# Optimization experiments

Hardware: AMD Instinct MI355X
Metric: run time of the kernel (lower is better)

The kernel has to match this reference:

```python
import jax, jax.numpy as jnp
import numpy as np
from jax import lax

D_MODEL = 1024
D_STATE = 16
D_CONV = 4
EXPAND = 2
D_INNER = EXPAND * D_MODEL           # 2048 (mamba inner)
DT_RANK = (D_MODEL + 15) // 16       # 64
D_FF = 4 * D_MODEL                   # 4096 (SwiGLU hidden)
EPS = 1e-5
B, L = 2, 2048


def setup_inputs() -> dict:
    key = jax.random.key(0)
    ks = jax.random.split(key, 16)
    s = 0.02
    inp = {
        'x': jax.random.normal(ks[0], (B, L, D_MODEL), jnp.float32),
        'norm1_w': jnp.ones((D_MODEL,), jnp.float32),
        'norm2_w': jnp.ones((D_MODEL,), jnp.float32),
        # Mamba params (torch Linear convention: y = x @ W.T)
        'in_proj_w': s * jax.random.normal(ks[1], (2 * D_INNER, D_MODEL), jnp.float32),
        'conv_w': s * jax.random.normal(ks[2], (D_INNER, 1, D_CONV), jnp.float32),
        'conv_b': jnp.zeros((D_INNER,), jnp.float32),
        'x_proj_w': s * jax.random.normal(ks[3], (DT_RANK + 2 * D_STATE, D_INNER), jnp.float32),
        'dt_proj_w': s * jax.random.normal(ks[4], (D_INNER, DT_RANK), jnp.float32),
        'dt_proj_b': jax.random.uniform(ks[5], (D_INNER,), jnp.float32, -4.0, -2.0),
        'A_log': jnp.log(jnp.broadcast_to(jnp.arange(1, D_STATE + 1, dtype=jnp.float32), (D_INNER, D_STATE))),
        'D': jnp.ones((D_INNER,), jnp.float32),
        'out_proj_w': s * jax.random.normal(ks[6], (D_MODEL, D_INNER), jnp.float32),
        # SwiGLU MLP
        'w1': s * jax.random.normal(ks[7], (D_FF, D_MODEL), jnp.float32),
        'w2': s * jax.random.normal(ks[8], (D_FF, D_MODEL), jnp.float32),
        'w3': s * jax.random.normal(ks[9], (D_MODEL, D_FF), jnp.float32),
    }
    return inp


def _rmsnorm(x, w, eps=EPS):
    return x * lax.rsqrt(jnp.mean(x * x, axis=-1, keepdims=True) + eps) * w


def _mamba(x, in_proj_w, conv_w, conv_b, x_proj_w, dt_proj_w, dt_proj_b, A_log, Dp, out_proj_w):
    # x: (B, L, d_model)
    xz = x @ in_proj_w.T                       # (B, L, 2*d_inner)
    u, z = jnp.split(xz, 2, axis=-1)           # each (B, L, d_inner)
    # causal depthwise conv1d over time
    u_nch = u.transpose(0, 2, 1)               # (B, d_inner, L)
    u_conv = lax.conv_general_dilated(
        u_nch, conv_w, window_strides=(1,), padding=[(D_CONV - 1, 0)],
        dimension_numbers=('NCH', 'OIH', 'NCH'), feature_group_count=D_INNER)
    u_conv = u_conv + conv_b[None, :, None]
    u_act = jax.nn.silu(u_conv.transpose(0, 2, 1))   # (B, L, d_inner)
    # input-dependent dt, B, C
    proj = u_act @ x_proj_w.T                  # (B, L, dt_rank + 2*d_state)
    dt_r, Bm, Cm = jnp.split(proj, [DT_RANK, DT_RANK + D_STATE], axis=-1)
    dt = jax.nn.softplus(dt_r @ dt_proj_w.T + dt_proj_b)   # (B, L, d_inner)
    A = -jnp.exp(A_log)                        # (d_inner, d_state)
    dA = jnp.exp(jnp.einsum('bld,dn->bldn', dt, A))
    dBu = jnp.einsum('bld,bln,bld->bldn', dt, Bm, u_act)
    def step(h, inputs):
        dA_t, dBu_t = inputs                   # (B, d_inner, d_state)
        h = dA_t * h + dBu_t
        return h, h
    h0 = jnp.zeros((x.shape[0], D_INNER, D_STATE), x.dtype)
    _, hs = lax.scan(step, h0, (dA.transpose(1, 0, 2, 3), dBu.transpose(1, 0, 2, 3)))
    y = jnp.einsum('lbdn,bln->bld', hs, Cm) + u_act * Dp   # (B, L, d_inner)
    y = y * jax.nn.silu(z)
    return y @ out_proj_w.T                    # (B, L, d_model)


def reference(x, norm1_w, norm2_w, in_proj_w, conv_w, conv_b, x_proj_w,
              dt_proj_w, dt_proj_b, A_log, D, out_proj_w, w1, w2, w3):
    # residual + RMSNorm + Mamba (dropout = eval-mode identity)
    h = x + _mamba(_rmsnorm(x, norm1_w), in_proj_w, conv_w, conv_b,
                   x_proj_w, dt_proj_w, dt_proj_b, A_log, D, out_proj_w)
    # residual + RMSNorm + SwiGLU MLP
    xn = _rmsnorm(h, norm2_w)
    mlp = (jax.nn.silu(xn @ w1.T) * (xn @ w2.T)) @ w3.T
    return h + mlp
```

## Files before the change

### kernel.cpp

```cpp
#include <hip/hip_runtime.h>
#include <hip/hip_bf16.h>

#define TOKS 4096
#define DM   1024
#define DI   2048
#define DST  16
#define DTR  64
#define DFF  4096
#define PROJ_LD 128

#define NC    32
#define CHUNK 64

typedef __bf16 bf16x8 __attribute__((ext_vector_type(8)));
typedef float  f32x4  __attribute__((ext_vector_type(4)));

__device__ __forceinline__ __bf16 f2bf(float f) {
  union { float f; unsigned u; } v; v.f = f;
  unsigned r = v.u + 0x7fffu + ((v.u >> 16) & 1u);
  union { unsigned short s; __bf16 b; } o; o.s = (unsigned short)(r >> 16);
  return o.b;
}
__device__ __forceinline__ float siluf(float x) { return x / (1.f + __expf(-x)); }
__device__ __forceinline__ float softplusf(float x) { return x > 20.f ? x : log1pf(__expf(x)); }

__device__ __forceinline__ void gl2lds16(const void* g, void* l) {
  __builtin_amdgcn_global_load_lds((const __attribute__((address_space(1))) void*)g,
                                   (__attribute__((address_space(3))) void*)l, 16, 0, 0);
}

struct CvtArgs {
  const float* src[5];
  __bf16*      dst[5];
  int nblk[6];
};

__global__ __launch_bounds__(256) void cvt_bf16_kernel(CvtArgs a) {
  int blk = blockIdx.x;
  int seg = 0;
#pragma unroll
  for (int s = 1; s < 5; s++) if (blk >= a.nblk[s]) seg = s;
  size_t base = (size_t)(blk - a.nblk[seg]) * 2048 + threadIdx.x * 8;
  const float* src = a.src[seg] + base;
  __bf16*      dst = a.dst[seg] + base;
  float4 v0 = *(const float4*)src;
  float4 v1 = *(const float4*)(src + 4);
  union { __bf16 b[8]; uint4 u; } t;
  t.b[0]=f2bf(v0.x); t.b[1]=f2bf(v0.y); t.b[2]=f2bf(v0.z); t.b[3]=f2bf(v0.w);
  t.b[4]=f2bf(v1.x); t.b[5]=f2bf(v1.y); t.b[6]=f2bf(v1.z); t.b[7]=f2bf(v1.w);
  *(uint4*)dst = t.u;
}

__global__ __launch_bounds__(256) void cvt_w12_kernel(const float* __restrict__ w1,
                                                      const float* __restrict__ w2,
                                                      __bf16* __restrict__ dst) {
  int blk = blockIdx.x;
  int isw2 = blk >> 11;
  int b = blk & 2047;
  int r = b * 2 + (threadIdx.x >> 7);
  int col = (threadIdx.x & 127) * 8;
  const float* src = (isw2 ? w2 : w1) + (size_t)r * DM + col;
  int dr = (r >> 4) * 32 + (r & 15) + isw2 * 16;
  float4 v0 = *(const float4*)src;
  float4 v1 = *(const float4*)(src + 4);
  union { __bf16 b[8]; uint4 u; } t;
  t.b[0]=f2bf(v0.x); t.b[1]=f2bf(v0.y); t.b[2]=f2bf(v0.z); t.b[3]=f2bf(v0.w);
  t.b[4]=f2bf(v1.x); t.b[5]=f2bf(v1.y); t.b[6]=f2bf(v1.z); t.b[7]=f2bf(v1.w);
  *(uint4*)&dst[(size_t)dr * DM + col] = t.u;
}

__global__ __launch_bounds__(256) void rmsnorm_kernel(const float* __restrict__ x,
                                                      const float* __restrict__ w,
                                                      __bf16* __restrict__ out) {
  int row = blockIdx.x;
  const float* xr = x + (size_t)row * DM;
  float4 v = ((const float4*)xr)[threadIdx.x];
  float ss = v.x*v.x + v.y*v.y + v.z*v.z + v.w*v.w;
#pragma unroll
  for (int o = 32; o > 0; o >>= 1) ss += __shfl_xor(ss, o);
  __shared__ float sred[4];
  if ((threadIdx.x & 63) == 0) sred[threadIdx.x >> 6] = ss;
  __syncthreads();
  float tot = sred[0] + sred[1] + sred[2] + sred[3];
  float scale = rsqrtf(tot * (1.f / DM) + 1e-5f);
  float4 wv = ((const float4*)w)[threadIdx.x];
  union { __bf16 b[4]; ushort4 u; } o;
  o.b[0] = f2bf(v.x * scale * wv.x);
  o.b[1] = f2bf(v.y * scale * wv.y);
  o.b[2] = f2bf(v.z * scale * wv.z);
  o.b[3] = f2bf(v.w * scale * wv.w);
  *(ushort4*)&out[(size_t)row * DM + threadIdx.x * 4] = o.u;
}

template<int BM, int EPI, int SWAP, int KK, int Z, int LDA, int LDB, int LDC>
__global__ __launch_bounds__(256, BM == 128 ? 1 : 2) void gemm2(
    const void* __restrict__ Ap, const __bf16* __restrict__ Bp,
    void* __restrict__ Cp, const void* __restrict__ auxp)
{
  constexpr int FM = BM / 32;
  constexpr int AI = BM / 64;
  constexpr int kPer = KK / Z;
  __shared__ __bf16 sA[2][BM * 32];
  __shared__ __bf16 sB[2][128 * 32];
  const int tid  = threadIdx.x;
  const int wave = tid >> 6, lane = tid & 63;
  const int bm = SWAP ? blockIdx.x : blockIdx.y;
  const int bn = SWAP ? blockIdx.y : blockIdx.x;
  const int m0 = bm * BM, n0 = bn * 128;
  const int wr = wave >> 1, wc = wave & 1;
  const int frow = lane & 15, fq = lane >> 4;

  f32x4 acc[FM][4] = {};

  const int kBeg = (Z > 1) ? blockIdx.z * kPer : 0;
  const int kEnd = kBeg + kPer;

  const int lrow = lane >> 2;
  const int lcol = (lane & 3) * 8;

  auto stage = [&](int kt, int buf) {
#pragma unroll
    for (int q = 0; q < AI; q++) {
      int idx = wave * AI + q;
      gl2lds16((const __bf16*)Ap + (size_t)(m0 + idx * 16 + lrow) * LDA + kt + lcol,
               &sA[buf][idx * 512]);
    }
#pragma unroll
    for (int q = 0; q < 2; q++) {
      int idx = wave * 2 + q;
      gl2lds16(Bp + (size_t)(n0 + idx * 16 + lrow) * LDB + kt + lcol,
               &sB[buf][idx * 512]);
    }
  };

  stage(kBeg, 0);
  int cur = 0;
  for (int kt = kBeg; kt < kEnd; kt += 32) {
    __syncthreads();

    bf16x8 afr[FM], bfr[4];
#pragma unroll
    for (int i = 0; i < FM; i++)
      afr[i] = *(const bf16x8*)&sA[cur][(wr * (BM/2) + i * 16 + frow) * 32 + fq * 8];
#pragma unroll
    for (int j = 0; j < 4; j++)
      bfr[j] = *(const bf16x8*)&sB[cur][(wc * 64 + j * 16 + frow) * 32 + fq * 8];

    if (kt + 32 < kEnd) stage(kt + 32, cur ^ 1);

#pragma unroll
    for (int i = 0; i < FM; i++)
#pragma unroll
      for (int j = 0; j < 4; j++)
        acc[i][j] = __builtin_amdgcn_mfma_f32_16x16x32_bf16(afr[i], bfr[j], acc[i][j], 0, 0, 0);
    cur ^= 1;
  }

  const float* auxf = (const float*)auxp;
#pragma unroll
  for (int i = 0; i < FM; i++) {
    int gr = m0 + wr * (BM/2) + i * 16 + fq * 4;
#pragma unroll
    for (int j = 0; j < 4; j++) {
      int gc = n0 + wc * 64 + j * 16 + frow;
#pragma unroll
      for (int r = 0; r < 4; r++) {
        float v = acc[i][j][r];
        if (EPI == 6) {
          if (j & 1) {
            int col = (n0 >> 1) + 32 * wc + 16 * (j >> 1) + frow;
            size_t off = (size_t)(gr + r) * LDC + col;
            float g = acc[i][j-1][r];
            ((__bf16*)Cp)[off] = f2bf(siluf(g) * v);
          }
        } else {
          size_t off = (size_t)(gr + r) * LDC + gc;
          if (EPI == 1) ((__bf16*)Cp)[off] = f2bf(v);
          else if (EPI == 2) ((__bf16*)Cp)[off] = f2bf(softplusf(v + auxf[gc]));
          else if (EPI == 3) ((float*)Cp)[off] = v + auxf[off];
          else if (EPI == 7)
            ((float*)Cp)[(size_t)blockIdx.z * (TOKS * PROJ_LD) + off] = v;
        }
      }
    }
  }
}

template<int EPI, int KK, int LDA, int LDB, int LDC, int GX>
__global__ __launch_bounds__(512, 2) void gemm8(
    const __bf16* __restrict__ Ap, const __bf16* __restrict__ Bp,
    void* __restrict__ Cp)
{
  constexpr int NT = KK / 64;
  static_assert(NT % 2 == 0 && NT >= 4, "KK must be a multiple of 128");
  __shared__ alignas(16) char S[131072];

  const int tid  = threadIdx.x;
  const int wid  = tid >> 6, lane = tid & 63;
  const int wr   = wid >> 2, wc = wid & 3;
  const int bid = blockIdx.y * (GX * 8) + blockIdx.x;
  const int xcd = bid & 7, idx = bid >> 3;
  const int m0 = (idx / GX) * 256;
  const int n0 = (xcd * GX + (idx % GX)) * 256;
  const int frow = lane & 15, fq = lane >> 4;
  const int cbyt = (fq * 16) ^ (((lane >> 3) & 1) << 5);
  const int srow = lane >> 2;
  const int skin = ((lane & 3) * 8) ^ (((lane >> 5) & 1) << 4);

  const unsigned sbase = (unsigned)(size_t)(__attribute__((address_space(3))) char*)S;
  const unsigned abase = sbase + (unsigned)((wr * 64 + frow) * 64 + cbyt);
  const unsigned bbase = sbase + 32768u + (unsigned)((wc * 32 + frow) * 64 + cbyt);

  f32x4 acc[2][2][4][2] = {};
  bf16x8 fA[4][2], fB0[2][2], fB1[2][2];

#define G8_SB() __builtin_amdgcn_sched_barrier(0)
#define G8_BAR() do { G8_SB(); __builtin_amdgcn_s_barrier(); G8_SB(); } while (0)
#define G8_LGKM0() do { asm volatile("s_waitcnt lgkmcnt(0)"); G8_SB(); } while (0)
#define G8_THROT() asm volatile("s_waitcnt lgkmcnt(8)")
#define G8_WAIT6() asm volatile("s_waitcnt vmcnt(6)")
#define G8_WAIT0() asm volatile("s_waitcnt vmcnt(0)")
#define G8_DSR(dst, addr, OFF)                                                 \
    asm volatile("ds_read_b128 %0, %1 offset:" OFF : "=v"(dst) : "v"(addr))

#define G8_STAGE(buf, ab, h, tile) do {                                        \
    if ((tile) < NT) {                                                         \
      const __bf16* gb = (ab) ? Bp : Ap;                                       \
      const int ld = (ab) ? LDB : LDA;                                         \
      const int r0 = ((ab) ? n0 : m0) + (h) * 128;                             \
      _Pragma("unroll")                                                        \
      for (int q = 0; q < 2; q++) {                                            \
        int p = wid * 2 + q, kk = p >> 3, r16 = p & 7;                         \
        const __bf16* src = gb + (size_t)(r0 + r16 * 16 + srow) * ld           \
                            + (tile) * 64 + kk * 32 + skin;                    \
        char* dst = S + (((buf) * 4 + (ab) * 2 + kk) << 14)                    \
                    + ((h) * 128 + r16 * 16) * 64;                             \
        gl2lds16(src, dst);                                                    \
      }                                                                        \
    }                                                                          \
  } while (0)

#define G8_READ_A(buf, mh) do {                                                \
    unsigned a_ = abase + (buf) * 65536u + (mh) * 8192u;                       \
    f32x4 t0,t1,t2,t3,t4,t5,t6,t7;                                             \
    G8_DSR(t0, a_, "0");     G8_DSR(t1, a_, "1024");                           \
    G8_DSR(t2, a_, "2048");  G8_DSR(t3, a_, "3072");                           \
    G8_DSR(t4, a_, "16384"); G8_DSR(t5, a_, "17408");                          \
    G8_DSR(t6, a_, "18432"); G8_DSR(t7, a_, "19456");                          \
    fA[0][0]=__builtin_bit_cast(bf16x8,t0); fA[1][0]=__builtin_bit_cast(bf16x8,t1); \
    fA[2][0]=__builtin_bit_cast(bf16x8,t2); fA[3][0]=__builtin_bit_cast(bf16x8,t3); \
    fA[0][1]=__builtin_bit_cast(bf16x8,t4); fA[1][1]=__builtin_bit_cast(bf16x8,t5); \
    fA[2][1]=__builtin_bit_cast(bf16x8,t6); fA[3][1]=__builtin_bit_cast(bf16x8,t7); \
  } while (0)

#define G8_READ_B(buf, nh, FB) do {                                            \
    unsigned b_ = bbase + (buf) * 65536u + (nh) * 8192u;                       \
    f32x4 t0,t1,t2,t3;                                                         \
    G8_DSR(t0, b_, "0");     G8_DSR(t1, b_, "1024");                           \
    G8_DSR(t2, b_, "16384"); G8_DSR(t3, b_, "17408");                          \
    FB[0][0]=__builtin_bit_cast(bf16x8,t0); FB[1][0]=__builtin_bit_cast(bf16x8,t1); \
    FB[0][1]=__builtin_bit_cast(bf16x8,t2); FB[1][1]=__builtin_bit_cast(bf16x8,t3); \
  } while (0)

#define G8_MFMA(mh, nh, FB) do {                                               \
    __builtin_amdgcn_s_setprio(1);                                             \
    _Pragma("unroll")                                                          \
    for (int kk = 0; kk < 2; kk++)                                             \
      _Pragma("unroll")                                                        \
      for (int fi = 0; fi < 4; fi++)                                           \
        _Pragma("unroll")                                                      \
        for (int fj = 0; fj < 2; fj++)                                         \
          acc[mh][nh][fi][fj] = __builtin_amdgcn_mfma_f32_16x16x32_bf16(       \
              fA[fi][kk], FB[fj][kk], acc[mh][nh][fi][fj], 0, 0, 0);           \
    __builtin_amdgcn_s_setprio(0);                                             \
    G8_SB();                                                                   \
  } while (0)

  G8_STAGE(0, 0, 0, 0); G8_STAGE(0, 1, 1, 0); G8_STAGE(0, 0, 1, 0); G8_STAGE(0, 1, 0, 0);
  G8_STAGE(1, 0, 0, 1); G8_STAGE(1, 1, 1, 1); G8_STAGE(1, 0, 1, 1);
  G8_SB();
  G8_WAIT6();
  G8_BAR();

  for (int it = 0; it < NT / 2; ++it) {
    const int t1 = 2 * it + 1, t2 = 2 * it + 2, t3 = 2 * it + 3;
    const bool last = (it == NT / 2 - 1);
    G8_READ_A(0, 0); G8_READ_B(0, 0, fB0);
    G8_STAGE(1, 1, 0, t1);
    G8_SB(); G8_THROT();
    G8_BAR();
    G8_LGKM0();
    G8_MFMA(0, 0, fB0);
    G8_BAR();
    G8_READ_B(0, 1, fB1);
    G8_STAGE(0, 0, 0, t2);
    G8_SB();
    G8_BAR();
    G8_LGKM0();
    G8_MFMA(0, 1, fB1);
    G8_BAR();
    G8_READ_A(0, 1);
    G8_STAGE(0, 1, 1, t2);
    G8_SB();
    G8_BAR();
    G8_LGKM0();
    G8_MFMA(1, 1, fB1);
    G8_BAR();
    G8_STAGE(0, 0, 1, t2);
    G8_SB();
    if (last) G8_WAIT0(); else G8_WAIT6();
    G8_BAR();
    G8_MFMA(1, 0, fB0);
    G8_BAR();
    G8_READ_A(1, 0); G8_READ_B(1, 0, fB0);
    G8_STAGE(0, 1, 0, t2);
    G8_SB(); G8_THROT();
    G8_BAR();
    G8_LGKM0();
    G8_MFMA(0, 0, fB0);
    G8_BAR();
    G8_READ_B(1, 1, fB1);
    G8_STAGE(1, 0, 0, t3);
    G8_SB();
    G8_BAR();
    G8_LGKM0();
    G8_MFMA(0, 1, fB1);
    G8_BAR();
    G8_READ_A(1, 1);
    G8_STAGE(1, 1, 1, t3);
    G8_SB();
    G8_BAR();
    G8_LGKM0();
    G8_MFMA(1, 1, fB1);
    G8_BAR();
    G8_STAGE(1, 0, 1, t3);
    G8_SB();
    if (!last) G8_WAIT6();
    G8_BAR();
    G8_MFMA(1, 0, fB0);
    G8_BAR();
  }

#undef G8_STAGE
#undef G8_READ_A
#undef G8_READ_B
#undef G8_MFMA
#undef G8_BAR
#undef G8_SB
#undef G8_LGKM0
#undef G8_THROT
#undef G8_WAIT6
#undef G8_WAIT0
#undef G8_DSR

#pragma unroll
  for (int mh = 0; mh < 2; mh++)
#pragma unroll
    for (int nh = 0; nh < 2; nh++)
#pragma unroll
      for (int fi = 0; fi < 4; fi++) {
        int gr = m0 + mh * 128 + wr * 64 + fi * 16 + fq * 4;
        if constexpr (EPI == 1) {
#pragma unroll
          for (int fj = 0; fj < 2; fj++) {
            int gc = n0 + nh * 128 + wc * 32 + fj * 16 + frow;
#pragma unroll
            for (int r = 0; r < 4; r++)
              ((__bf16*)Cp)[(size_t)(gr + r) * LDC + gc] = f2bf(acc[mh][nh][fi][fj][r]);
          }
        } else {
          int col = ((n0 + nh * 128 + wc * 32) >> 1) + frow;
#pragma unroll
          for (int r = 0; r < 4; r++) {
            float g = acc[mh][nh][fi][0][r];
            float v = acc[mh][nh][fi][1][r];
            ((__bf16*)Cp)[(size_t)(gr + r) * LDC + col] = f2bf(siluf(g) * v);
          }
        }
      }
}

__global__ __launch_bounds__(256) void xp_reduce_kernel(const float* __restrict__ part,
                                                        float* __restrict__ proj,
                                                        __bf16* __restrict__ projb) {
  int i = blockIdx.x * 256 + threadIdx.x;
  float4 s = ((const float4*)part)[i];
#pragma unroll
  for (int z = 1; z < 8; z++) {
    float4 v = ((const float4*)(part + (size_t)z * TOKS * PROJ_LD))[i];
    s.x += v.x; s.y += v.y; s.z += v.z; s.w += v.w;
  }
  ((float4*)proj)[i] = s;
  int c4 = i & 31;
  if (c4 < 16) {
    int tok = i >> 5;
    union { __bf16 b[4]; ushort4 u; } t;
    t.b[0]=f2bf(s.x); t.b[1]=f2bf(s.y); t.b[2]=f2bf(s.z); t.b[3]=f2bf(s.w);
    *(ushort4*)&projb[(size_t)tok * 64 + c4 * 4] = t.u;
  }
}

__global__ __launch_bounds__(256) void conv_silu_kernel(const __bf16* __restrict__ xz,
                                                        const float* __restrict__ cw,
                                                        const float* __restrict__ cb,
                                                        __bf16* __restrict__ uact) {
  int idx = blockIdx.x * 256 + threadIdx.x;
  int d8  = (idx & 255) * 8;
  int tok = idx >> 8;
  int l   = tok & 2047;
  const __bf16* up = xz + (size_t)tok * (2 * DI) + d8;
  bf16x8 u0 = {}, u1 = {}, u2 = {}, u3;
  if (l >= 3) u0 = *(const bf16x8*)(up - 3 * (2 * DI));
  if (l >= 2) u1 = *(const bf16x8*)(up - 2 * (2 * DI));
  if (l >= 1) u2 = *(const bf16x8*)(up - 1 * (2 * DI));
  u3 = *(const bf16x8*)up;
  float4 cb0 = *(const float4*)(cb + d8);
  float4 cb1 = *(const float4*)(cb + d8 + 4);
  float cbv[8] = {cb0.x, cb0.y, cb0.z, cb0.w, cb1.x, cb1.y, cb1.z, cb1.w};
  union { __bf16 b[8]; uint4 u; } res;
#pragma unroll
  for (int j = 0; j < 8; j++) {
    float4 wv = *(const float4*)(cw + (size_t)(d8 + j) * 4);
    float acc = cbv[j];
    acc += wv.x * (float)u0[j];
    acc += wv.y * (float)u1[j];
    acc += wv.z * (float)u2[j];
    acc += wv.w * (float)u3[j];
    res.b[j] = f2bf(siluf(acc));
  }
  *(uint4*)&uact[(size_t)tok * DI + d8] = res.u;
}

__global__ __launch_bounds__(64) void scan_pass1(const __bf16* __restrict__ dt,
                                                 const __bf16* __restrict__ uact,
                                                 const float* __restrict__ proj,
                                                 const float* __restrict__ A_log,
                                                 float* __restrict__ aprod,
                                                 float* __restrict__ hend) {
  int lane = threadIdx.x;
  int d = blockIdx.x * 64 + lane;
  int c = blockIdx.y, b = blockIdx.z;
  float An[16], h[16], ap[16];
  {
    const float4* a4 = (const float4*)(A_log + (size_t)d * 16);
#pragma unroll
    for (int q = 0; q < 4; q++) {
      float4 v = a4[q];
      An[q*4+0] = -__expf(v.x); An[q*4+1] = -__expf(v.y);
      An[q*4+2] = -__expf(v.z); An[q*4+3] = -__expf(v.w);
    }
  }
#pragma unroll
  for (int n = 0; n < 16; n++) { h[n] = 0.f; ap[n] = 1.f; }

  size_t tok = (size_t)b * 2048 + (size_t)c * CHUNK;
  const __bf16* dtp = dt   + tok * DI + d;
  const __bf16* up  = uact + tok * DI + d;
  const float*  pp  = proj + tok * PROJ_LD;

  for (int t = 0; t < CHUNK; t++) {
    float dtv = (float)*dtp;
    float uv  = (float)*up;
    const float4* b4 = (const float4*)(pp + 64);
    float Bv[16];
#pragma unroll
    for (int q = 0; q < 4; q++) {
      float4 v = b4[q];
      Bv[q*4+0]=v.x; Bv[q*4+1]=v.y; Bv[q*4+2]=v.z; Bv[q*4+3]=v.w;
    }
    float du = dtv * uv;
#pragma unroll
    for (int n = 0; n < 16; n++) {
      float dA = __expf(dtv * An[n]);
      ap[n] *= dA;
      h[n] = fmaf(dA, h[n], du * Bv[n]);
    }
    dtp += DI; up += DI; pp += PROJ_LD;
  }

  size_t off = ((size_t)(b * NC + c) * DI + d) * 16;
#pragma unroll
  for (int q = 0; q < 4; q++) {
    *(float4*)(hend  + off + q*4) = make_float4(h[q*4+0],  h[q*4+1],  h[q*4+2],  h[q*4+3]);
    *(float4*)(aprod + off + q*4) = make_float4(ap[q*4+0], ap[q*4+1], ap[q*4+2], ap[q*4+3]);
  }
}

__global__ __launch_bounds__(256) void scan_pass2(const float* __restrict__ aprod,
                                                  const float* __restrict__ hend,
                                                  float* __restrict__ hstart) {
  int idx = blockIdx.x * 256 + threadIdx.x;
  int b  = idx >> 13;
  int r4 = idx & 8191;
  float4 H = make_float4(0.f, 0.f, 0.f, 0.f);
  for (int c = 0; c < NC; c++) {
    size_t off = (size_t)(b * NC + c) * (DI * 16 / 4) + r4;
    ((float4*)hstart)[off] = H;
    float4 a = ((const float4*)aprod)[off];
    float4 e = ((const float4*)hend)[off];
    H.x = fmaf(a.x, H.x, e.x);
    H.y = fmaf(a.y, H.y, e.y);
    H.z = fmaf(a.z, H.z, e.z);
    H.w = fmaf(a.w, H.w, e.w);
  }
}

__global__ __launch_bounds__(64) void scan_pass3(const __bf16* __restrict__ dt,
                                                 const __bf16* __restrict__ uact,
                                                 const float* __restrict__ proj,
                                                 const __bf16* __restrict__ xz,
                                                 const float* __restrict__ A_log,
                                                 const float* __restrict__ Dp,
                                                 const float* __restrict__ hstart,
                                                 __bf16* __restrict__ y) {
  int lane = threadIdx.x;
  int d = blockIdx.x * 64 + lane;
  int c = blockIdx.y, b = blockIdx.z;
  float An[16], h[16];
  {
    const float4* a4 = (const float4*)(A_log + (size_t)d * 16);
#pragma unroll
    for (int q = 0; q < 4; q++) {
      float4 v = a4[q];
      An[q*4+0] = -__expf(v.x); An[q*4+1] = -__expf(v.y);
      An[q*4+2] = -__expf(v.z); An[q*4+3] = -__expf(v.w);
    }
  }
  {
    size_t off = ((size_t)(b * NC + c) * DI + d) * 16;
#pragma unroll
    for (int q = 0; q < 4; q++) {
      float4 v = *(const float4*)(hstart + off + q*4);
      h[q*4+0]=v.x; h[q*4+1]=v.y; h[q*4+2]=v.z; h[q*4+3]=v.w;
    }
  }
  float Dd = Dp[d];

  size_t tok = (size_t)b * 2048 + (size_t)c * CHUNK;
  const __bf16* dtp = dt   + tok * DI + d;
  const __bf16* up  = uact + tok * DI + d;
  const float*  pp  = proj + tok * PROJ_LD;
  const __bf16* zp  = xz   + tok * (2 * DI) + DI + d;
  __bf16*       yp  = y    + tok * DI + d;

  for (int t = 0; t < CHUNK; t++) {
    float dtv = (float)*dtp;
    float uv  = (float)*up;
    float zv  = (float)*zp;
    const float4* b4 = (const float4*)(pp + 64);
    float Bv[16], Cv[16];
#pragma unroll
    for (int q = 0; q < 4; q++) {
      float4 v = b4[q];
      Bv[q*4+0]=v.x; Bv[q*4+1]=v.y; Bv[q*4+2]=v.z; Bv[q*4+3]=v.w;
      float4 w = b4[q + 4];
      Cv[q*4+0]=w.x; Cv[q*4+1]=w.y; Cv[q*4+2]=w.z; Cv[q*4+3]=w.w;
    }
    float du = dtv * uv;
    float p = 0.f;
#pragma unroll
    for (int n = 0; n < 16; n++) {
      float dA = __expf(dtv * An[n]);
      h[n] = fmaf(dA, h[n], du * Bv[n]);
      p = fmaf(h[n], Cv[n], p);
    }
    *yp = f2bf((p + Dd * uv) * siluf(zv));
    dtp += DI; up += DI; pp += PROJ_LD; zp += 2 * DI; yp += DI;
  }
}

extern "C" void kernel_launch(void* const* d_in, const int* in_sizes, int n_in,
                              void* d_out, int out_size, void* d_ws, size_t ws_size,
                              hipStream_t stream) {
  const float* x        = (const float*)d_in[0];
  const float* n1w      = (const float*)d_in[1];
  const float* n2w      = (const float*)d_in[2];
  const float* in_projw = (const float*)d_in[3];
  const float* conv_w   = (const float*)d_in[4];
  const float* conv_b   = (const float*)d_in[5];
  const float* x_projw  = (const float*)d_in[6];
  const float* dt_projw = (const float*)d_in[7];
  const float* dt_projb = (const float*)d_in[8];
  const float* A_log    = (const float*)d_in[9];
  const float* Dp       = (const float*)d_in[10];
  const float* out_projw= (const float*)d_in[11];
  const float* w1       = (const float*)d_in[12];
  const float* w2       = (const float*)d_in[13];
  const float* w3       = (const float*)d_in[14];
  float* out = (float*)d_out;

  char* ws = (char*)d_ws;
  __bf16* xz   = (__bf16*)(ws + 0);
  __bf16* uact = (__bf16*)(ws + 33554432);
  float*  proj = (float*) (ws + 50331648);
  __bf16* dt   = (__bf16*)(ws + 52428800);
  __bf16* yb   = (__bf16*)(ws + 85983232);
  float*  xpp  = (float*) (ws + 85983232);
  float*  h    = (float*) (ws + 102760448);
  __bf16* xn   = (__bf16*)(ws + 119537664);
  __bf16* hid  = xz;
  __bf16* projb = (__bf16*)(ws + 102760448);
  float* aprod  = (float*)(ws + 102760448);
  float* hend   = (float*)(ws + 111149056);
  float* hstart = (float*)(ws + 119537664);
  char* wb = ws + 127926272;
  __bf16* b_in  = (__bf16*)(wb);
  __bf16* b_xp  = (__bf16*)(wb + 8388608);
  __bf16* b_dtp = (__bf16*)(wb + 8912896);
  __bf16* b_out = (__bf16*)(wb + 9175040);
  __bf16* b_w12 = (__bf16*)(wb + 13369344);
  __bf16* b_w3  = (__bf16*)(wb + 30146560);

  hipMemsetAsync(b_xp, 0, 128 * 2048 * sizeof(__bf16), stream);

  CvtArgs ca;
  const float* srcs[5] = {in_projw, x_projw, dt_projw, out_projw, w3};
  __bf16* dsts[5]      = {b_in, b_xp, b_dtp, b_out, b_w3};
  int counts[5] = {4096*1024, 96*2048, 2048*64, 1024*2048, 1024*4096};
  int acc = 0;
  for (int i = 0; i < 5; i++) { ca.src[i] = srcs[i]; ca.dst[i] = dsts[i]; ca.nblk[i] = acc; acc += counts[i] / 2048; }
  ca.nblk[5] = acc;
  cvt_bf16_kernel<<<acc, 256, 0, stream>>>(ca);
  cvt_w12_kernel<<<4096, 256, 0, stream>>>(w1, w2, b_w12);

  dim3 blk(256);
  rmsnorm_kernel<<<TOKS, 256, 0, stream>>>(x, n1w, xn);
  gemm8<1, 1024, DM, DM, 4096, 2><<<dim3(16, 16), 512, 0, stream>>>(xn, b_in, xz);
  conv_silu_kernel<<<(TOKS*DI/8)/256, 256, 0, stream>>>(xz, conv_w, conv_b, uact);
  gemm2<64,7,0, 2048,8, DI,DI,PROJ_LD><<<dim3(1,64,8), blk, 0, stream>>>(uact, b_xp, xpp, nullptr);
  xp_reduce_kernel<<<512, 256, 0, stream>>>(xpp, proj, projb);
  gemm2<128,2,0, 64,1, 64,DTR,DI><<<dim3(16,32,1), blk, 0, stream>>>(projb, b_dtp, dt, dt_projb);
  scan_pass1<<<dim3(DI/64, NC, 2), 64, 0, stream>>>(dt, uact, proj, A_log, aprod, hend);
  scan_pass2<<<64, 256, 0, stream>>>(aprod, hend, hstart);
  scan_pass3<<<dim3(DI/64, NC, 2), 64, 0, stream>>>(dt, uact, proj, xz, A_log, Dp, hstart, yb);
  gemm2<64,3,1, 2048,1, DI,DI,DM><<<dim3(64,8,1), blk, 0, stream>>>(yb, b_out, h, x);
  rmsnorm_kernel<<<TOKS, 256, 0, stream>>>(h, n2w, xn);
  gemm8<6, 1024, DM, DM, DFF, 4><<<dim3(32, 16), 512, 0, stream>>>(xn, b_w12, hid);
  gemm2<64,3,1, 4096,1, DFF,DFF,DM><<<dim3(64,8,1), blk, 0, stream>>>(hid, b_w3, out, h);

  (void)in_sizes; (void)n_in; (void)out_size; (void)ws_size;
}
```

Measured before the change: 524.4 us.

## Add 4-stage async-LDS pipelined GEMM for out_proj and w3 residual GEMMs

After: 509.5 us. -2.8%, faster.

```diff
diff --git a/kernel.cpp b/kernel.cpp
--- a/kernel.cpp
+++ b/kernel.cpp
@@ -166,21 +166,108 @@
 #pragma unroll
       for (int r = 0; r < 4; r++) {
         float v = acc[i][j][r];
-        if (EPI == 6) {
-          if (j & 1) {
-            int col = (n0 >> 1) + 32 * wc + 16 * (j >> 1) + frow;
-            size_t off = (size_t)(gr + r) * LDC + col;
-            float g = acc[i][j-1][r];
-            ((__bf16*)Cp)[off] = f2bf(siluf(g) * v);
-          }
-        } else {
-          size_t off = (size_t)(gr + r) * LDC + gc;
-          if (EPI == 1) ((__bf16*)Cp)[off] = f2bf(v);
-          else if (EPI == 2) ((__bf16*)Cp)[off] = f2bf(softplusf(v + auxf[gc]));
-          else if (EPI == 3) ((float*)Cp)[off] = v + auxf[off];
-          else if (EPI == 7)
-            ((float*)Cp)[(size_t)blockIdx.z * (TOKS * PROJ_LD) + off] = v;
-        }
+        size_t off = (size_t)(gr + r) * LDC + gc;
+        if (EPI == 1) ((__bf16*)Cp)[off] = f2bf(v);
+        else if (EPI == 2) ((__bf16*)Cp)[off] = f2bf(softplusf(v + auxf[gc]));
+        else if (EPI == 3) ((float*)Cp)[off] = v + auxf[off];
+        else if (EPI == 7)
+          ((float*)Cp)[(size_t)blockIdx.z * (TOKS * PROJ_LD) + off] = v;
+      }
+    }
+  }
+}
+
+template<int KK, int LDA, int LDB, int LDC>
+__global__ __launch_bounds__(256, 2) void gemm2d(
+    const __bf16* __restrict__ Ap, const __bf16* __restrict__ Bp,
+    float* __restrict__ Cp, const float* __restrict__ auxp)
+{
+  constexpr int NSTEP = KK / 32;
+  static_assert(NSTEP % 4 == 0 && NSTEP >= 8, "KK must be mult of 128");
+  __shared__ alignas(16) char S2[49152];
+  const int tid  = threadIdx.x;
+  const int wave = tid >> 6, lane = tid & 63;
+  const int m0 = blockIdx.x * 64, n0 = blockIdx.y * 128;
+  const int wr = wave >> 1, wc = wave & 1;
+  const int frow = lane & 15, fq = lane >> 4;
+  const int lrow = lane >> 2, lcol = (lane & 3) * 8;
+
+  f32x4 acc[2][4] = {};
+
+  const unsigned s2 = (unsigned)(size_t)(__attribute__((address_space(3))) char*)S2;
+  const unsigned aAddr = s2 + (unsigned)((wr * 32 + frow) * 64 + fq * 16);
+  const unsigned bAddr = s2 + 16384u + (unsigned)((wc * 64 + frow) * 64 + fq * 16);
+
+  auto stage = [&](int tile, int buf) {
+    gl2lds16(Ap + (size_t)(m0 + wave * 16 + lrow) * LDA + tile * 32 + lcol,
+             S2 + buf * 4096 + wave * 1024);
+#pragma unroll
+    for (int q = 0; q < 2; q++) {
+      int idx = wave * 2 + q;
+      gl2lds16(Bp + (size_t)(n0 + idx * 16 + lrow) * LDB + tile * 32 + lcol,
+               S2 + 16384 + buf * 8192 + idx * 1024);
+    }
+  };
+
+#define D_SB() __builtin_amdgcn_sched_barrier(0)
+#define D_DSR(dst, addr, OFF)                                                  \
+    asm volatile("ds_read_b128 %0, %1 offset:" OFF : "=v"(dst) : "v"(addr))
+#define D_STEP(t, B, OA0, OA1, OB0, OB1, OB2, OB3)                             \
+  do {                                                                         \
+    if ((t) + 3 < NSTEP) stage((t) + 3, ((B) + 3) & 3);                        \
+    D_SB();                                                                    \
+    if ((t) + 3 < NSTEP)      asm volatile("s_waitcnt vmcnt(9)");              \
+    else if ((t) + 2 < NSTEP) asm volatile("s_waitcnt vmcnt(6)");              \
+    else if ((t) + 1 < NSTEP) asm volatile("s_waitcnt vmcnt(3)");              \
+    else                      asm volatile("s_waitcnt vmcnt(0)");              \
+    D_SB();                                                                    \
+    __builtin_amdgcn_s_barrier();              \
+    D_SB();                                                                    \
+    f32x4 ta0, ta1, tb0, tb1, tb2, tb3;                                        \
+    D_DSR(ta0, aAddr, OA0); D_DSR(ta1, aAddr, OA1);                            \
+    D_DSR(tb0, bAddr, OB0); D_DSR(tb1, bAddr, OB1);                            \
+    D_DSR(tb2, bAddr, OB2); D_DSR(tb3, bAddr, OB3);                            \
+    asm volatile("s_waitcnt lgkmcnt(0)");                                      \
+    D_SB();                                                                    \
+    __builtin_amdgcn_s_barrier();           \
+    D_SB();                                                                    \
+    bf16x8 a0 = __builtin_bit_cast(bf16x8, ta0);                               \
+    bf16x8 a1 = __builtin_bit_cast(bf16x8, ta1);                               \
+    bf16x8 b0 = __builtin_bit_cast(bf16x8, tb0);                               \
+    bf16x8 b1 = __builtin_bit_cast(bf16x8, tb1);                               \
+    bf16x8 b2 = __builtin_bit_cast(bf16x8, tb2);                               \
+    bf16x8 b3 = __builtin_bit_cast(bf16x8, tb3);                               \
+    acc[0][0] = __builtin_amdgcn_mfma_f32_16x16x32_bf16(a0, b0, acc[0][0], 0, 0, 0); \
+    acc[0][1] = __builtin_amdgcn_mfma_f32_16x16x32_bf16(a0, b1, acc[0][1], 0, 0, 0); \
+    acc[0][2] = __builtin_amdgcn_mfma_f32_16x16x32_bf16(a0, b2, acc[0][2], 0, 0, 0); \
+    acc[0][3] = __builtin_amdgcn_mfma_f32_16x16x32_bf16(a0, b3, acc[0][3], 0, 0, 0); \
+    acc[1][0] = __builtin_amdgcn_mfma_f32_16x16x32_bf16(a1, b0, acc[1][0], 0, 0, 0); \
+    acc[1][1] = __builtin_amdgcn_mfma_f32_16x16x32_bf16(a1, b1, acc[1][1], 0, 0, 0); \
+    acc[1][2] = __builtin_amdgcn_mfma_f32_16x16x32_bf16(a1, b2, acc[1][2], 0, 0, 0); \
+    acc[1][3] = __builtin_amdgcn_mfma_f32_16x16x32_bf16(a1, b3, acc[1][3], 0, 0, 0); \
+  } while (0)
+
+  stage(0, 0); stage(1, 1); stage(2, 2);
+  for (int t = 0; t < NSTEP; t += 4) {
+    D_STEP(t + 0, 0, "0",     "1024",  "0",     "1024",  "2048",  "3072");
+    D_STEP(t + 1, 1, "4096",  "5120",  "8192",  "9216",  "10240", "11264");
+    D_STEP(t + 2, 2, "8192",  "9216",  "16384", "17408", "18432", "19456");
+    D_STEP(t + 3, 3, "12288", "13312", "24576", "25600", "26624", "27648");
+  }
+#undef D_STEP
+#undef D_DSR
+#undef D_SB
+
+#pragma unroll
+  for (int i = 0; i < 2; i++) {
+    int gr = m0 + wr * 32 + i * 16 + fq * 4;
+#pragma unroll
+    for (int j = 0; j < 4; j++) {
+      int gc = n0 + wc * 64 + j * 16 + frow;
+#pragma unroll
+      for (int r = 0; r < 4; r++) {
+        size_t off = (size_t)(gr + r) * LDC + gc;
+        Cp[off] = acc[i][j][r] + auxp[off];
       }
     }
   }
@@ -633,10 +720,10 @@
   scan_pass1<<<dim3(DI/64, NC, 2), 64, 0, stream>>>(dt, uact, proj, A_log, aprod, hend);
   scan_pass2<<<64, 256, 0, stream>>>(aprod, hend, hstart);
   scan_pass3<<<dim3(DI/64, NC, 2), 64, 0, stream>>>(dt, uact, proj, xz, A_log, Dp, hstart, yb);
-  gemm2<64,3,1, 2048,1, DI,DI,DM><<<dim3(64,8,1), blk, 0, stream>>>(yb, b_out, h, x);
+  gemm2d<2048, DI, DI, DM><<<dim3(64, 8), blk, 0, stream>>>(yb, b_out, h, x);
   rmsnorm_kernel<<<TOKS, 256, 0, stream>>>(h, n2w, xn);
   gemm8<6, 1024, DM, DM, DFF, 4><<<dim3(32, 16), 512, 0, stream>>>(xn, b_w12, hid);
-  gemm2<64,3,1, 4096,1, DFF,DFF,DM><<<dim3(64,8,1), blk, 0, stream>>>(hid, b_w3, out, h);
+  gemm2d<4096, DFF, DFF, DM><<<dim3(64, 8), blk, 0, stream>>>(hid, b_w3, out, h);
 
   (void)in_sizes; (void)n_in; (void)out_size; (void)ws_size;
 }
```
